# Kernel optimization log

Measured on AMD Instinct MI355X. Metric: run time of the kernel, lower is better.

Reference implementation:

```python
import jax, jax.numpy as jnp
import numpy as np
import math

D = 512; H = 8; L = 6; FF = 2048; S = 512; B = 32; IN = 64; OUT = 1
HD = D // H
EPS = 1e-5


def _pos_encoding(seq_len, d_model):
    position = jnp.arange(seq_len, dtype=jnp.float32)[:, None]
    div_term = jnp.exp(jnp.arange(0, d_model, 2, dtype=jnp.float32) * (-math.log(10000.0) / d_model))
    ang = position * div_term  # [S, D/2]
    pe = jnp.zeros((seq_len, d_model), dtype=jnp.float32)
    pe = pe.at[:, 0::2].set(jnp.sin(ang)).at[:, 1::2].set(jnp.cos(ang))
    return pe


def _layernorm(x, g, b):
    m = jnp.mean(x, axis=-1, keepdims=True)
    v = jnp.mean((x - m) ** 2, axis=-1, keepdims=True)
    return (x - m) * jax.lax.rsqrt(v + EPS) * g + b


def setup_inputs() -> dict:
    key = jax.random.key(0)
    ks = jax.random.split(key, 20)
    s = 0.02
    return {
        "src": jax.random.normal(ks[0], (B, S, IN), dtype=jnp.float32),
        "inp_w": jax.random.uniform(ks[1], (D, IN), minval=-0.1, maxval=0.1, dtype=jnp.float32),
        "inp_b": jnp.zeros((D,), dtype=jnp.float32),
        "in_proj_w": jax.random.normal(ks[2], (L, 3 * D, D), dtype=jnp.float32) * s,
        "in_proj_b": jnp.zeros((L, 3 * D), dtype=jnp.float32),
        "out_w": jax.random.normal(ks[3], (L, D, D), dtype=jnp.float32) * s,
        "out_b": jnp.zeros((L, D), dtype=jnp.float32),
        "ff_w1": jax.random.normal(ks[4], (L, FF, D), dtype=jnp.float32) * s,
        "ff_b1": jnp.zeros((L, FF), dtype=jnp.float32),
        "ff_w2": jax.random.normal(ks[5], (L, D, FF), dtype=jnp.float32) * s,
        "ff_b2": jnp.zeros((L, D), dtype=jnp.float32),
        "ln1_g": jnp.ones((L, D), dtype=jnp.float32),
        "ln1_b": jnp.zeros((L, D), dtype=jnp.float32),
        "ln2_g": jnp.ones((L, D), dtype=jnp.float32),
        "ln2_b": jnp.zeros((L, D), dtype=jnp.float32),
        "op_w1": jax.random.normal(ks[6], (FF, D), dtype=jnp.float32) * s,
        "op_b1": jnp.zeros((FF,), dtype=jnp.float32),
        "op_w2": jax.random.normal(ks[7], (OUT, FF), dtype=jnp.float32) * s,
        "op_b2": jnp.zeros((OUT,), dtype=jnp.float32),
    }


def reference(src, inp_w, inp_b, in_proj_w, in_proj_b, out_w, out_b,
              ff_w1, ff_b1, ff_w2, ff_b2, ln1_g, ln1_b, ln2_g, ln2_b,
              op_w1, op_b1, op_w2, op_b2):
    # input projection + sqrt(d_model) scale + positional encoding
    x = (src @ inp_w.T + inp_b) * math.sqrt(D)
    x = x + _pos_encoding(S, D)[None, :, :]
    scale = 1.0 / math.sqrt(HD)
    for i in range(L):
        # self-attention (torch nn.MultiheadAttention, eval mode, no mask)
        qkv = x @ in_proj_w[i].T + in_proj_b[i]            # [B,S,3D]
        q, k, v = jnp.split(qkv, 3, axis=-1)
        q = q.reshape(B, S, H, HD).transpose(0, 2, 1, 3)   # [B,H,S,HD]
        k = k.reshape(B, S, H, HD).transpose(0, 2, 1, 3)
        v = v.reshape(B, S, H, HD).transpose(0, 2, 1, 3)
        scores = jnp.einsum('bhqd,bhkd->bhqk', q, k) * scale
        attn = jax.nn.softmax(scores, axis=-1)             # [B,H,S,S]
        o = jnp.einsum('bhqk,bhkd->bhqd', attn, v)
        o = o.transpose(0, 2, 1, 3).reshape(B, S, D)
        o = o @ out_w[i].T + out_b[i]
        x = _layernorm(x + o, ln1_g[i], ln1_b[i])
        # feedforward
        h = jax.nn.relu(x @ ff_w1[i].T + ff_b1[i])
        ff = h @ ff_w2[i].T + ff_b2[i]
        x = _layernorm(x + ff, ln2_g[i], ln2_b[i])
    # take last timestep, output projection MLP
    last = x[:, -1, :]                                     # [B,D]
    h = jax.nn.relu(last @ op_w1.T + op_b1)
    return h @ op_w2.T + op_b2                             # [B,OUT]
```

## Files before the change

kernel.cpp:

```cpp
#include <hip/hip_runtime.h>

typedef short s16x8 __attribute__((ext_vector_type(8)));
typedef float f32x4 __attribute__((ext_vector_type(4)));
typedef float f32x16 __attribute__((ext_vector_type(16)));

__device__ short g_wbuf[18874368];
__device__ short g_srcb[1048576];
__device__ short g_inpwb[32768];
__device__ float g_pe[262144];
__device__ float g_hpart[256];

__device__ inline float b2f(short s) {
  union { unsigned int u; float f; } v;
  v.u = ((unsigned int)(unsigned short)s) << 16;
  return v.f;
}
__device__ inline short f2b(float f) {
  union { float f; unsigned int u; } v; v.f = f;
  unsigned int r = (v.u + 0x7fffu + ((v.u >> 16) & 1u)) >> 16;
  return (short)r;
}
__device__ inline s16x8 pack8(float4 a, float4 b) {
  s16x8 r;
  r[0] = f2b(a.x); r[1] = f2b(a.y); r[2] = f2b(a.z); r[3] = f2b(a.w);
  r[4] = f2b(b.x); r[5] = f2b(b.y); r[6] = f2b(b.z); r[7] = f2b(b.w);
  return r;
}

__device__ inline f32x4 mfma16(s16x8 a, s16x8 b, f32x4 c) {
  return __builtin_amdgcn_mfma_f32_16x16x32_bf16(a, b, c, 0, 0, 0);
}
__device__ inline f32x16 mfma32(s16x8 a, s16x8 b, f32x16 c) {
  return __builtin_amdgcn_mfma_f32_32x32x16_bf16(a, b, c, 0, 0, 0);
}

typedef const __attribute__((address_space(1))) void* as1cptr;
typedef __attribute__((address_space(3))) void* as3ptr;
__device__ inline void gl2lds16(const short* g, short* l) {
  __builtin_amdgcn_global_load_lds((as1cptr)g, (as3ptr)l, 16, 0, 0);
}

__global__ void __launch_bounds__(256)
cvt2_kernel(const float* __restrict__ i0, const float* __restrict__ i1) {
  const int b = blockIdx.x;
  const float* src; short* dst; int base;
  if (b < 512) { src = i0; dst = g_srcb; base = b; }
  else         { src = i1; dst = g_inpwb; base = b - 512; }
  const int idx = (base * 256 + threadIdx.x) * 8;
  float4 a = *(const float4*)(src + idx);
  float4 c = *(const float4*)(src + idx + 4);
  *(s16x8*)(dst + idx) = pack8(a, c);
}

__global__ void __launch_bounds__(256)
cvt6_kernel(const float* __restrict__ i0, const float* __restrict__ i1,
            const float* __restrict__ i2, const float* __restrict__ i3) {
  const int b = blockIdx.x;
  const float* src; short* dst; int base;
  if (b < 2304)      { src = i0; dst = g_wbuf;            base = b; }
  else if (b < 3072) { src = i1; dst = g_wbuf +  4718592; base = b - 2304; }
  else if (b < 6144) { src = i2; dst = g_wbuf +  6291456; base = b - 3072; }
  else               { src = i3; dst = g_wbuf + 12582912; base = b - 6144; }
  const int idx = (base * 256 + threadIdx.x) * 8;
  float4 a = *(const float4*)(src + idx);
  float4 c = *(const float4*)(src + idx + 4);
  *(s16x8*)(dst + idx) = pack8(a, c);
}

__global__ void __launch_bounds__(256)
pe_kernel() {
  const int s = blockIdx.x;
  const int n0 = threadIdx.x * 2;
  const float ang = (float)s * expf((float)n0 * -0.0179889460390160f);
  g_pe[s * 512 + n0]     = sinf(ang);
  g_pe[s * 512 + n0 + 1] = cosf(ang);
}

template <int EPI>
__global__ void __launch_bounds__(256, 3)
gemm_bt(const short* __restrict__ Ain, int woff, const float* __restrict__ bias,
        short* __restrict__ C, int M, int N, int K) {
  __shared__ short As[128 * 64];
  __shared__ short Bs[128 * 64];
  const int tid  = threadIdx.x;
  const int lane = tid & 63;
  const int wave = tid >> 6;
  const int wr = (wave >> 1) << 6;
  const int wc = (wave & 1) << 6;
  const int l31 = lane & 31;
  const int half = lane >> 5;
  const int bm = blockIdx.x & 127;
  const int bn = blockIdx.x >> 7;

  const short* A = (EPI == 2) ? (const short*)g_srcb : Ain;
  const short* W = (EPI == 2) ? (const short*)g_inpwb : (const short*)(g_wbuf + woff);

  int srow[4], soff[4];
#pragma unroll
  for (int i = 0; i < 4; ++i) {
    const int u = i * 256 + tid;
    srow[i] = u >> 3;
    soff[i] = ((u & 7) ^ ((u >> 3) & 7)) << 3;
  }
  const int rsw = lane & 7;
  f32x16 acc[2][2] = {};

  for (int k0 = 0; k0 < K; k0 += 64) {
#pragma unroll
    for (int i = 0; i < 4; ++i) {
      gl2lds16(A + (size_t)(bm * 128 + srow[i]) * K + k0 + soff[i],
               As + (i * 256 + tid) * 8);
      gl2lds16(W + (size_t)(bn * 128 + srow[i]) * K + k0 + soff[i],
               Bs + (i * 256 + tid) * 8);
    }
    __syncthreads();
#pragma unroll
    for (int ks = 0; ks < 4; ++ks) {
      const int rchunk = ((ks * 2 + half) ^ rsw) * 8;
      s16x8 af[2], bfr[2];
#pragma unroll
      for (int i = 0; i < 2; ++i)
        af[i] = *(const s16x8*)(As + (wr + i * 32 + l31) * 64 + rchunk);
#pragma unroll
      for (int j = 0; j < 2; ++j)
        bfr[j] = *(const s16x8*)(Bs + (wc + j * 32 + l31) * 64 + rchunk);
#pragma unroll
      for (int i = 0; i < 2; ++i)
#pragma unroll
        for (int j = 0; j < 2; ++j)
          acc[i][j] = mfma32(af[i], bfr[j], acc[i][j]);
    }
    __syncthreads();
  }

#pragma unroll
  for (int j = 0; j < 2; ++j) {
    const int col = bn * 128 + wc + j * 32 + l31;
    const float bv = bias[col];
#pragma unroll
    for (int i = 0; i < 2; ++i) {
      const int rbase = bm * 128 + wr + i * 32 + half * 4;
#pragma unroll
      for (int r = 0; r < 16; ++r) {
        const int row = rbase + (r & 3) + 8 * (r >> 2);
        float v = acc[i][j][r] + bv;
        if (EPI == 1) v = fmaxf(v, 0.0f);
        if (EPI == 2) {
          const int s = row & 511;
          v = (acc[i][j][r] + bv) * 22.62741699796952f + g_pe[s * 512 + col];
        }
        C[(size_t)row * N + col] = f2b(v);
      }
    }
  }
}

__global__ void __launch_bounds__(512, 4)
attn_kernel(const short* __restrict__ qkv, short* __restrict__ ctx) {
  __shared__ short KV[2][8192];
  __shared__ short Pt[8192];
  __shared__ float rcomb[2][4][16];
  const int tid = threadIdx.x;
  const int lane = tid & 63, wave = tid >> 6;
  const int ml = lane & 15, quad = lane >> 4;
  const int mt = wave >> 1, nh = wave & 1;
  const int qt = (blockIdx.x >> 3) & 7;
  const int bh = (blockIdx.x & 7) | ((blockIdx.x >> 6) << 3);
  const int b = bh >> 3, h = bh & 7;
  const size_t basebs = (size_t)b * 512 * 1536;
  const int hoff = h * 64;

  s16x8 qf0, qf1;
  {
    const int qrow = qt * 64 + mt * 16 + ml;
    const short* qp = qkv + basebs + (size_t)qrow * 1536 + hoff;
    qf0 = *(const s16x8*)(qp + quad * 8);
    qf1 = *(const s16x8*)(qp + 32 + quad * 8);
  }

  const int srow0 = tid >> 3, srow1 = srow0 + 64;
  const int soff0 = (((tid & 7) ^ (srow0 & 7)) << 3);
  const int soff1 = (((tid & 7) ^ (srow1 & 7)) << 3);
  const short* kbase = qkv + basebs + 512 + hoff;

  const int vkp = tid & 63, vd8 = (tid >> 6) << 3;
  const short* vbase = qkv + basebs + 1024 + hoff + vd8;
  s16x8 va, vb;

  gl2lds16(kbase + (size_t)srow0 * 1536 + soff0, &KV[0][tid * 8]);
  gl2lds16(kbase + (size_t)srow1 * 1536 + soff1, &KV[0][(512 + tid) * 8]);
  __syncthreads();

  f32x4 sc[4][4];
#pragma unroll
  for (int rr = 0; rr < 4; ++rr) {
    if (rr < 3) {
      const short* kb = kbase + (size_t)((rr + 1) * 128) * 1536;
      short* dst = &KV[(rr + 1) & 1][0];
      gl2lds16(kb + (size_t)srow0 * 1536 + soff0, dst + tid * 8);
      gl2lds16(kb + (size_t)srow1 * 1536 + soff1, dst + (512 + tid) * 8);
    } else {
      const short* vp = vbase + (size_t)(vkp * 2) * 1536;
      va = *(const s16x8*)vp;
      vb = *(const s16x8*)(vp + 1536);
    }
    const short* kbuf = &KV[rr & 1][0];
#pragma unroll
    for (int nt = 0; nt < 4; ++nt) {
      const int krow = nh * 64 + nt * 16 + ml;
      const short* kr = kbuf + krow * 64;
      s16x8 kf0 = *(const s16x8*)(kr + ((quad ^ (ml & 7)) << 3));
      s16x8 kf1 = *(const s16x8*)(kr + (((quad + 4) ^ (ml & 7)) << 3));
      f32x4 s0 = {};
      s0 = mfma16(qf0, kf0, s0);
      s0 = mfma16(qf1, kf1, s0);
      sc[rr][nt] = s0;
    }
    if (rr == 3) {
      short* vt = &KV[0][0];
#pragma unroll
      for (int j = 0; j < 8; ++j) {
        const int d = vd8 + j;
        unsigned int u = (unsigned int)(unsigned short)va[j]
                       | ((unsigned int)(unsigned short)vb[j] << 16);
        *(unsigned int*)(vt + d * 128 + ((((vkp >> 2) ^ (d & 15)) << 3) | ((vkp & 3) << 1))) = u;
      }
    }
    __syncthreads();
  }

  float rm[4];
  {
    f32x4 rmx = sc[0][0];
#pragma unroll
    for (int rr = 0; rr < 4; ++rr)
#pragma unroll
      for (int nt = 0; nt < 4; ++nt)
#pragma unroll
        for (int r = 0; r < 4; ++r)
          rmx[r] = fmaxf(rmx[r], sc[rr][nt][r]);
#pragma unroll
    for (int off = 1; off <= 8; off <<= 1)
#pragma unroll
      for (int r = 0; r < 4; ++r)
        rmx[r] = fmaxf(rmx[r], __shfl_xor(rmx[r], off));
    if (ml == 0) {
#pragma unroll
      for (int r = 0; r < 4; ++r)
        rcomb[nh][mt][quad * 4 + r] = rmx[r];
    }
    __syncthreads();
#pragma unroll
    for (int r = 0; r < 4; ++r)
      rm[r] = 0.125f * fmaxf(rcomb[0][mt][quad * 4 + r], rcomb[1][mt][quad * 4 + r]);
  }

  f32x4 oacc[2] = {};
  float psum[4] = {0.f, 0.f, 0.f, 0.f};
#pragma unroll
  for (int rr = 0; rr < 4; ++rr) {
    if (rr < 3) {
      const short* vp = vbase + (size_t)((rr + 1) * 128 + vkp * 2) * 1536;
      va = *(const s16x8*)vp;
      vb = *(const s16x8*)(vp + 1536);
    }
#pragma unroll
    for (int nt = 0; nt < 4; ++nt) {
#pragma unroll
      for (int r = 0; r < 4; ++r) {
        float p = __expf(sc[rr][nt][r] * 0.125f - rm[r]);
        short pb = f2b(p);
        psum[r] += b2f(pb);
        const int qrl = mt * 16 + quad * 4 + r;
        const int c = nh * 64 + nt * 16 + ml;
        Pt[qrl * 128 + ((((c >> 3) ^ (qrl & 15)) << 3) | (c & 7))] = pb;
      }
    }
    __syncthreads();
    const short* vbuf = &KV[rr & 1][0];
    const int prow = mt * 16 + ml;
#pragma unroll
    for (int ks = 0; ks < 4; ++ks) {
      s16x8 pf = *(const s16x8*)(Pt + prow * 128 + ((((ks << 2) | quad) ^ ml) << 3));
#pragma unroll
      for (int n2 = 0; n2 < 2; ++n2) {
        const int nd = (nh * 2 + n2) * 16 + ml;
        s16x8 vf = *(const s16x8*)(vbuf + nd * 128 + ((((ks << 2) | quad) ^ ml) << 3));
        oacc[n2] = mfma16(pf, vf, oacc[n2]);
      }
    }
    if (rr < 3) {
      short* vt = &KV[(rr + 1) & 1][0];
#pragma unroll
      for (int j = 0; j < 8; ++j) {
        const int d = vd8 + j;
        unsigned int u = (unsigned int)(unsigned short)va[j]
                       | ((unsigned int)(unsigned short)vb[j] << 16);
        *(unsigned int*)(vt + d * 128 + ((((vkp >> 2) ^ (d & 15)) << 3) | ((vkp & 3) << 1))) = u;
      }
    }
    __syncthreads();
  }

#pragma unroll
  for (int off = 1; off <= 8; off <<= 1)
#pragma unroll
    for (int r = 0; r < 4; ++r)
      psum[r] += __shfl_xor(psum[r], off);
  if (ml == 0) {
#pragma unroll
    for (int r = 0; r < 4; ++r)
      rcomb[nh][mt][quad * 4 + r] = psum[r];
  }
  __syncthreads();

#pragma unroll
  for (int r = 0; r < 4; ++r) {
    const float l = rcomb[0][mt][quad * 4 + r] + rcomb[1][mt][quad * 4 + r];
    const float rl = 1.0f / l;
    const int grow = qt * 64 + mt * 16 + quad * 4 + r;
#pragma unroll
    for (int n2 = 0; n2 < 2; ++n2) {
      const int d = (nh * 2 + n2) * 16 + ml;
      ctx[((size_t)b * 512 + grow) * 512 + hoff + d] = f2b(oacc[n2][r] * rl);
    }
  }
}

__global__ void __launch_bounds__(256)
ln_kernel(short* __restrict__ x, const short* __restrict__ o,
          const float* __restrict__ g, const float* __restrict__ bta) {
  const int row = blockIdx.x * 4 + (threadIdx.x >> 6);
  const int lane = threadIdx.x & 63;
  short* xp = x + (size_t)row * 512 + lane * 8;
  const short* op = o + (size_t)row * 512 + lane * 8;
  s16x8 xv = *(const s16x8*)xp;
  s16x8 ov = *(const s16x8*)op;
  float v[8]; float s = 0.f, s2 = 0.f;
#pragma unroll
  for (int e = 0; e < 8; ++e) {
    float f = b2f(xv[e]) + b2f(ov[e]);
    v[e] = f; s += f; s2 += f * f;
  }
#pragma unroll
  for (int off = 32; off >= 1; off >>= 1) {
    s += __shfl_xor(s, off);
    s2 += __shfl_xor(s2, off);
  }
  const float mean = s * (1.f / 512.f);
  const float var = s2 * (1.f / 512.f) - mean * mean;
  const float rstd = rsqrtf(var + 1e-5f);
  float4 g0 = *(const float4*)(g + lane * 8);
  float4 g1 = *(const float4*)(g + lane * 8 + 4);
  float4 b0 = *(const float4*)(bta + lane * 8);
  float4 b1 = *(const float4*)(bta + lane * 8 + 4);
  float gv[8] = {g0.x, g0.y, g0.z, g0.w, g1.x, g1.y, g1.z, g1.w};
  float bv[8] = {b0.x, b0.y, b0.z, b0.w, b1.x, b1.y, b1.z, b1.w};
  s16x8 outv;
#pragma unroll
  for (int e = 0; e < 8; ++e)
    outv[e] = f2b((v[e] - mean) * rstd * gv[e] + bv[e]);
  *(s16x8*)xp = outv;
}

__global__ void __launch_bounds__(256)
head1_kernel(const short* __restrict__ x, const float* __restrict__ w1,
             const float* __restrict__ b1, const float* __restrict__ w2) {
  const int bidx = blockIdx.x;
  const int b = bidx >> 3, seg = bidx & 7;
  const int tid = threadIdx.x;
  __shared__ float xl[512];
  __shared__ float red[256];
  for (int n = tid; n < 512; n += 256)
    xl[n] = b2f(x[((size_t)b * 512 + 511) * 512 + n]);
  __syncthreads();
  const int f = seg * 256 + tid;
  const float* wr = w1 + (size_t)f * 512;
  float hv = 0.f;
  for (int k8 = 0; k8 < 64; ++k8) {
    float4 wa = *(const float4*)(wr + k8 * 8);
    float4 wb = *(const float4*)(wr + k8 * 8 + 4);
    hv += xl[k8 * 8 + 0] * wa.x + xl[k8 * 8 + 1] * wa.y +
          xl[k8 * 8 + 2] * wa.z + xl[k8 * 8 + 3] * wa.w +
          xl[k8 * 8 + 4] * wb.x + xl[k8 * 8 + 5] * wb.y +
          xl[k8 * 8 + 6] * wb.z + xl[k8 * 8 + 7] * wb.w;
  }
  hv += b1[f];
  hv = fmaxf(hv, 0.f);
  red[tid] = hv * w2[f];
  __syncthreads();
  for (int stride = 128; stride > 0; stride >>= 1) {
    if (tid < stride) red[tid] += red[tid + stride];
    __syncthreads();
  }
  if (tid == 0) g_hpart[bidx] = red[0];
}

__global__ void __launch_bounds__(64)
head2_kernel(const float* __restrict__ b2, float* __restrict__ out) {
  const int t = threadIdx.x;
  if (t < 32) {
    float s = 0.f;
#pragma unroll
    for (int c = 0; c < 8; ++c) s += g_hpart[t * 8 + c];
    out[t] = s + b2[0];
  }
}

extern "C" void kernel_launch(void* const* d_in, const int* in_sizes, int n_in,
                              void* d_out, int out_size, void* d_ws, size_t ws_size,
                              hipStream_t stream) {
  (void)in_sizes; (void)n_in; (void)out_size; (void)ws_size;
  const float* src       = (const float*)d_in[0];
  const float* inp_w     = (const float*)d_in[1];
  const float* inp_b     = (const float*)d_in[2];
  const float* in_proj_w = (const float*)d_in[3];
  const float* in_proj_b = (const float*)d_in[4];
  const float* out_w     = (const float*)d_in[5];
  const float* out_b     = (const float*)d_in[6];
  const float* ff_w1     = (const float*)d_in[7];
  const float* ff_b1     = (const float*)d_in[8];
  const float* ff_w2     = (const float*)d_in[9];
  const float* ff_b2     = (const float*)d_in[10];
  const float* ln1_g     = (const float*)d_in[11];
  const float* ln1_b     = (const float*)d_in[12];
  const float* ln2_g     = (const float*)d_in[13];
  const float* ln2_b     = (const float*)d_in[14];
  const float* op_w1     = (const float*)d_in[15];
  const float* op_b1     = (const float*)d_in[16];
  const float* op_w2     = (const float*)d_in[17];
  const float* op_b2     = (const float*)d_in[18];

  short* ws   = (short*)d_ws;
  short* x    = ws;
  short* qkv  = ws + 8388608;
  short* ctx  = qkv + 25165824;
  short* obuf = ctx + 8388608;
  short* h    = qkv;

  cvt2_kernel<<<528, 256, 0, stream>>>(src, inp_w);
  cvt6_kernel<<<9216, 256, 0, stream>>>(in_proj_w, out_w, ff_w1, ff_w2);
  pe_kernel<<<512, 256, 0, stream>>>();
  gemm_bt<2><<<512, 256, 0, stream>>>(nullptr, 0, inp_b, x, 16384, 512, 64);

  for (int l = 0; l < 6; ++l) {
    const int w_qkv = l * 786432;
    const int w_out = 4718592 + l * 262144;
    const int w_ff1 = 6291456 + l * 1048576;
    const int w_ff2 = 12582912 + l * 1048576;
    gemm_bt<0><<<1536, 256, 0, stream>>>(
        x, w_qkv, in_proj_b + l * 1536, qkv, 16384, 1536, 512);
    attn_kernel<<<2048, 512, 0, stream>>>(qkv, ctx);
    gemm_bt<0><<<512, 256, 0, stream>>>(
        ctx, w_out, out_b + l * 512, obuf, 16384, 512, 512);
    ln_kernel<<<4096, 256, 0, stream>>>(x, obuf, ln1_g + l * 512, ln1_b + l * 512);
    gemm_bt<1><<<2048, 256, 0, stream>>>(
        x, w_ff1, ff_b1 + l * 2048, h, 16384, 2048, 512);
    gemm_bt<0><<<512, 256, 0, stream>>>(
        h, w_ff2, ff_b2 + l * 512, obuf, 16384, 512, 2048);
    ln_kernel<<<4096, 256, 0, stream>>>(x, obuf, ln2_g + l * 512, ln2_b + l * 512);
  }
  head1_kernel<<<256, 256, 0, stream>>>(x, op_w1, op_b1, op_w2);
  head2_kernel<<<1, 64, 0, stream>>>(op_b2, (float*)d_out);
}
```

Measured before the change: 1.524 ms.

## Convert attention to single-pass online softmax with per-tile V transpose

The attention kernel no longer runs a separate QK pass storing all scores, a global max reduction, then a PV pass. It now computes scores, a running max and rescaling, and PV per 128-key tile in one loop. K stays double-buffered and V gets its own transposed LDS buffer. This cuts score register pressure (16 f32x4 down to 4), which may allow higher occupancy, but adds rescale exps, per-tile max syncs, and V loads that are no longer prefetched a tile ahead.

Result: slower. 1.688 ms (+10.7%).

```diff
diff --git a/kernel.cpp b/kernel.cpp
--- a/kernel.cpp
+++ b/kernel.cpp
@@ -157,7 +157,8 @@
 
 __global__ void __launch_bounds__(512, 4)
 attn_kernel(const short* __restrict__ qkv, short* __restrict__ ctx) {
-  __shared__ short KV[2][8192];
+  __shared__ short Kb[2][8192];
+  __shared__ short VT[8192];
   __shared__ short Pt[8192];
   __shared__ float rcomb[2][4][16];
   const int tid = threadIdx.x;
@@ -185,26 +186,29 @@
 
   const int vkp = tid & 63, vd8 = (tid >> 6) << 3;
   const short* vbase = qkv + basebs + 1024 + hoff + vd8;
-  s16x8 va, vb;
-
-  gl2lds16(kbase + (size_t)srow0 * 1536 + soff0, &KV[0][tid * 8]);
-  gl2lds16(kbase + (size_t)srow1 * 1536 + soff1, &KV[0][(512 + tid) * 8]);
+
+  gl2lds16(kbase + (size_t)srow0 * 1536 + soff0, &Kb[0][tid * 8]);
+  gl2lds16(kbase + (size_t)srow1 * 1536 + soff1, &Kb[0][(512 + tid) * 8]);
   __syncthreads();
 
-  f32x4 sc[4][4];
+  f32x4 oacc[2] = {};
+  float psum[4] = {0.f, 0.f, 0.f, 0.f};
+  float mrun[4] = {-1e30f, -1e30f, -1e30f, -1e30f};
+
 #pragma unroll
   for (int rr = 0; rr < 4; ++rr) {
     if (rr < 3) {
-      const short* kb = kbase + (size_t)((rr + 1) * 128) * 1536;
-      short* dst = &KV[(rr + 1) & 1][0];
-      gl2lds16(kb + (size_t)srow0 * 1536 + soff0, dst + tid * 8);
-      gl2lds16(kb + (size_t)srow1 * 1536 + soff1, dst + (512 + tid) * 8);
-    } else {
-      const short* vp = vbase + (size_t)(vkp * 2) * 1536;
-      va = *(const s16x8*)vp;
-      vb = *(const s16x8*)(vp + 1536);
-    }
-    const short* kbuf = &KV[rr & 1][0];
+      const short* kb2 = kbase + (size_t)((rr + 1) * 128) * 1536;
+      short* dst = &Kb[(rr + 1) & 1][0];
+      gl2lds16(kb2 + (size_t)srow0 * 1536 + soff0, dst + tid * 8);
+      gl2lds16(kb2 + (size_t)srow1 * 1536 + soff1, dst + (512 + tid) * 8);
+    }
+    const short* vp = vbase + (size_t)(rr * 128 + vkp * 2) * 1536;
+    s16x8 va = *(const s16x8*)vp;
+    s16x8 vb = *(const s16x8*)(vp + 1536);
+
+    const short* kbuf = &Kb[rr & 1][0];
+    f32x4 sc[4];
 #pragma unroll
     for (int nt = 0; nt < 4; ++nt) {
       const int krow = nh * 64 + nt * 16 + ml;
@@ -214,61 +218,52 @@
       f32x4 s0 = {};
       s0 = mfma16(qf0, kf0, s0);
       s0 = mfma16(qf1, kf1, s0);
-      sc[rr][nt] = s0;
-    }
-    if (rr == 3) {
-      short* vt = &KV[0][0];
-#pragma unroll
-      for (int j = 0; j < 8; ++j) {
-        const int d = vd8 + j;
-        unsigned int u = (unsigned int)(unsigned short)va[j]
-                       | ((unsigned int)(unsigned short)vb[j] << 16);
-        *(unsigned int*)(vt + d * 128 + ((((vkp >> 2) ^ (d & 15)) << 3) | ((vkp & 3) << 1))) = u;
-      }
-    }
-    __syncthreads();
-  }
-
-  float rm[4];
-  {
-    f32x4 rmx = sc[0][0];
-#pragma unroll
-    for (int rr = 0; rr < 4; ++rr)
-#pragma unroll
-      for (int nt = 0; nt < 4; ++nt)
-#pragma unroll
-        for (int r = 0; r < 4; ++r)
-          rmx[r] = fmaxf(rmx[r], sc[rr][nt][r]);
+      sc[nt] = s0;
+    }
+
+#pragma unroll
+    for (int j = 0; j < 8; ++j) {
+      const int d = vd8 + j;
+      unsigned int u = (unsigned int)(unsigned short)va[j]
+                     | ((unsigned int)(unsigned short)vb[j] << 16);
+      *(unsigned int*)(VT + d * 128 + ((((vkp >> 2) ^ (d & 15)) << 3) | ((vkp & 3) << 1))) = u;
+    }
+
+    f32x4 tmx = sc[0];
+#pragma unroll
+    for (int nt = 1; nt < 4; ++nt)
+#pragma unroll
+      for (int r = 0; r < 4; ++r)
+        tmx[r] = fmaxf(tmx[r], sc[nt][r]);
 #pragma unroll
     for (int off = 1; off <= 8; off <<= 1)
 #pragma unroll
       for (int r = 0; r < 4; ++r)
-        rmx[r] = fmaxf(rmx[r], __shfl_xor(rmx[r], off));
+        tmx[r] = fmaxf(tmx[r], __shfl_xor(tmx[r], off));
     if (ml == 0) {
 #pragma unroll
       for (int r = 0; r < 4; ++r)
-        rcomb[nh][mt][quad * 4 + r] = rmx[r];
-    }
-    __syncthreads();
-#pragma unroll
-    for (int r = 0; r < 4; ++r)
-      rm[r] = 0.125f * fmaxf(rcomb[0][mt][quad * 4 + r], rcomb[1][mt][quad * 4 + r]);
-  }
-
-  f32x4 oacc[2] = {};
-  float psum[4] = {0.f, 0.f, 0.f, 0.f};
-#pragma unroll
-  for (int rr = 0; rr < 4; ++rr) {
-    if (rr < 3) {
-      const short* vp = vbase + (size_t)((rr + 1) * 128 + vkp * 2) * 1536;
-      va = *(const s16x8*)vp;
-      vb = *(const s16x8*)(vp + 1536);
-    }
+        rcomb[nh][mt][quad * 4 + r] = tmx[r];
+    }
+    __syncthreads();
+
+#pragma unroll
+    for (int r = 0; r < 4; ++r) {
+      const float tm = 0.125f * fmaxf(rcomb[0][mt][quad * 4 + r],
+                                      rcomb[1][mt][quad * 4 + r]);
+      const float mn = fmaxf(mrun[r], tm);
+      const float scl = __expf(mrun[r] - mn);
+      mrun[r] = mn;
+      psum[r] *= scl;
+      oacc[0][r] *= scl;
+      oacc[1][r] *= scl;
+    }
+
 #pragma unroll
     for (int nt = 0; nt < 4; ++nt) {
 #pragma unroll
       for (int r = 0; r < 4; ++r) {
-        float p = __expf(sc[rr][nt][r] * 0.125f - rm[r]);
+        float p = __expf(sc[nt][r] * 0.125f - mrun[r]);
         short pb = f2b(p);
         psum[r] += b2f(pb);
         const int qrl = mt * 16 + quad * 4 + r;
@@ -277,7 +272,7 @@
       }
     }
     __syncthreads();
-    const short* vbuf = &KV[rr & 1][0];
+
     const int prow = mt * 16 + ml;
 #pragma unroll
     for (int ks = 0; ks < 4; ++ks) {
@@ -285,18 +280,8 @@
 #pragma unroll
       for (int n2 = 0; n2 < 2; ++n2) {
         const int nd = (nh * 2 + n2) * 16 + ml;
-        s16x8 vf = *(const s16x8*)(vbuf + nd * 128 + ((((ks << 2) | quad) ^ ml) << 3));
+        s16x8 vf = *(const s16x8*)(VT + nd * 128 + ((((ks << 2) | quad) ^ ml) << 3));
         oacc[n2] = mfma16(pf, vf, oacc[n2]);
-      }
-    }
-    if (rr < 3) {
-      short* vt = &KV[(rr + 1) & 1][0];
-#pragma unroll
-      for (int j = 0; j < 8; ++j) {
-        const int d = vd8 + j;
-        unsigned int u = (unsigned int)(unsigned short)va[j]
-                       | ((unsigned int)(unsigned short)vb[j] << 16);
-        *(unsigned int*)(vt + d * 128 + ((((vkp >> 2) ^ (d & 15)) << 3) | ((vkp & 3) << 1))) = u;
       }
     }
     __syncthreads();
```
